# Optimization experiments

Hardware: AMD Instinct MI355X
Metric: run time of the kernel (lower is better)

## Reference

```python
import jax, jax.numpy as jnp
import numpy as np

N = 400_000
B = 64          # number of segments (point clouds)
IN_C = 128
INTER = (256, 512, 512)
OUT_C = 512


def setup_inputs() -> dict:
    key = jax.random.key(0)
    ks = jax.random.split(key, 12)
    pos_emd = jax.random.normal(ks[0], (N, IN_C), dtype=jnp.float32)
    radius_p_batch = jnp.sort(jax.random.randint(ks[1], (N,), 0, B))

    def lin(k, fin, fout):
        kw, kb = jax.random.split(k)
        s = 1.0 / np.sqrt(fin)
        W = jax.random.uniform(kw, (fin, fout), jnp.float32, -s, s)
        b = jax.random.uniform(kb, (fout,), jnp.float32, -s, s)
        return W, b

    W1, b1 = lin(ks[2], IN_C, INTER[0])
    W2, b2 = lin(ks[3], INTER[0], INTER[1])
    W3, b3 = lin(ks[4], INTER[1], INTER[2])
    W4, b4 = lin(ks[5], IN_C + INTER[2], OUT_C)
    W5, b5 = lin(ks[6], OUT_C, OUT_C)
    return {
        "pos_emd": pos_emd, "radius_p_batch": radius_p_batch,
        "W1": W1, "b1": b1, "W2": W2, "b2": b2, "W3": W3, "b3": b3,
        "W4": W4, "b4": b4, "W5": W5, "b5": b5,
    }


def reference(pos_emd, radius_p_batch, W1, b1, W2, b2, W3, b3, W4, b4, W5, b5):
    # mlp1: Linear-ReLU-Linear-ReLU-Linear
    h = jax.nn.relu(pos_emd @ W1 + b1)
    h = jax.nn.relu(h @ W2 + b2)
    h = h @ W3 + b3                              # [N, 512]
    # global max pool over segments
    g = jax.ops.segment_max(h, radius_p_batch, num_segments=B)  # [B, 512]
    # broadcast each segment's global feature back to its points (ids sorted)
    g_rep = g[radius_p_batch]                    # [N, 512]
    z = jnp.concatenate((pos_emd, g_rep), axis=-1)  # [N, 640]
    # mlp2: Linear-ReLU-Linear
    z = jax.nn.relu(z @ W4 + b4)
    z = z @ W5 + b5                              # [N, 512]
    return jax.ops.segment_max(z, radius_p_batch, num_segments=B)  # [B, 512]
```

## Files before the change

kernel.cpp:

```cpp
#include <hip/hip_runtime.h>
#include <stdint.h>


typedef __bf16 bf16;
typedef __bf16 bf16x4 __attribute__((ext_vector_type(4)));
typedef __bf16 bf16x8 __attribute__((ext_vector_type(8)));
typedef float f32x4 __attribute__((ext_vector_type(4)));

#define N_PTS 400000
#define ORD_NEG_INF 0x007FFFFFu

__device__ __forceinline__ unsigned f2ord(float f) {
  unsigned u = __float_as_uint(f);
  return (u & 0x80000000u) ? ~u : (u | 0x80000000u);
}
__device__ __forceinline__ float ord2f(unsigned o) {
  unsigned u = (o & 0x80000000u) ? (o ^ 0x80000000u) : ~o;
  return __uint_as_float(u);
}

__device__ __forceinline__ void gld16(const bf16* g, bf16* l) {
  __builtin_amdgcn_global_load_lds((const __attribute__((address_space(1))) void*)g,
                                   (__attribute__((address_space(3))) void*)l, 16, 0, 0);
}

__global__ void k_init(unsigned* g_ord, unsigned* out_u) {
  int i = blockIdx.x * 256 + threadIdx.x;
  if (i < 64 * 512) { g_ord[i] = ORD_NEG_INF; out_u[i] = ORD_NEG_INF; }
}

__global__ void k_convX(const float* __restrict__ x, bf16* __restrict__ y, long n4) {
  long i = (long)blockIdx.x * 256 + threadIdx.x;
  long stride = (long)gridDim.x * 256;
  for (; i < n4; i += stride) {
    float4 v = ((const float4*)x)[i];
    bf16x4 o = {(bf16)v.x, (bf16)v.y, (bf16)v.z, (bf16)v.w};
    ((bf16x4*)y)[i] = o;
  }
}

__global__ void k_convWt(const float* __restrict__ W, bf16* __restrict__ Wt, int K, int Nout) {
  int idx = blockIdx.x * 256 + threadIdx.x;
  if (idx < K * Nout) {
    int k = idx / Nout, c = idx - k * Nout;
    Wt[(size_t)c * K + k] = (bf16)W[idx];
  }
}

__global__ void k_segbias(const unsigned* __restrict__ g_ord, const float* __restrict__ W4,
                          const float* __restrict__ b4, float* __restrict__ sb) {
  const int s = blockIdx.x, c = threadIdx.x;
  __shared__ float gs[512];
  gs[c] = ord2f(g_ord[s * 512 + c]);
  __syncthreads();
  float acc = b4[c];
  for (int j = 0; j < 512; ++j) acc = fmaf(gs[j], W4[(size_t)(128 + j) * 512 + c], acc);
  sb[s * 512 + c] = acc;
}

__global__ void k_decode(unsigned* p, int n) {
  int i = blockIdx.x * 256 + threadIdx.x;
  if (i < n) { float f = ord2f(p[i]); ((float*)p)[i] = f; }
}

template <int BIASMODE, bool RELU, int EPI, int K, int NOUT>
__launch_bounds__(256)
__global__ void k_gemm(const bf16* __restrict__ A, const bf16* __restrict__ Bt,
                       const float* __restrict__ bias, const int* __restrict__ ids,
                       long row_off, bf16* __restrict__ out,
                       unsigned* __restrict__ outAtomic) {
  constexpr int KT = K / 32;
  constexpr int NBX = NOUT / 128;
  __shared__ __align__(16) bf16 sA[2][4096];
  __shared__ __align__(16) bf16 sB[2][4096];
  __shared__ int sIds[128];
  const int tid = threadIdx.x;
  const int wid = tid >> 6, lane = tid & 63;

  const int nwg = NBX * (int)gridDim.y;
  const int orig = (int)blockIdx.y * NBX + (int)blockIdx.x;
  const int q = nwg >> 3, r = nwg & 7;
  const int xcd = orig & 7, lid = orig >> 3;
  const int wg = (xcd < r ? xcd * (q + 1) : r * (q + 1) + (xcd - r) * q) + lid;
  const int n0 = (wg % NBX) * 128;
  const int m0 = (wg / NBX) * 128;

  if ((BIASMODE == 1 || EPI == 1) && tid < 128) sIds[tid] = ids[row_off + m0 + tid];

  const int c0 = wid * 64 + lane;
  const int srow = c0 >> 2;
  const int schunk = (c0 & 3) ^ ((c0 >> 3) & 3);
  const bf16* gA0 = A + (size_t)(m0 + srow) * K + schunk * 8;
  const bf16* gA1 = gA0 + (size_t)64 * K;
  const bf16* gB0 = Bt + (size_t)(n0 + srow) * K + schunk * 8;
  const bf16* gB1 = gB0 + (size_t)64 * K;
  bf16* sA0 = &sA[0][0];
  bf16* sB0 = &sB[0][0];

  auto STAGE = [&](int b, int kt) {
    const int ko = kt * 32;
    bf16* la = sA0 + b * 4096 + wid * 512;
    bf16* lb = sB0 + b * 4096 + wid * 512;
    gld16(gA0 + ko, la); gld16(gA1 + ko, la + 2048);
    gld16(gB0 + ko, lb); gld16(gB1 + ko, lb + 2048);
  };

  const int wr = wid >> 1, wc = wid & 1;
  const int lr = lane & 15, lk = lane >> 4;
  const int swz = (lr >> 1) & 3;
  const int foA = (wr * 64 + lr) * 32 + ((lk ^ swz) * 8);
  const int foB = (wc * 64 + lr) * 32 + ((lk ^ swz) * 8);

  f32x4 acc[4][4];
#pragma unroll
  for (int i = 0; i < 4; ++i)
#pragma unroll
    for (int j = 0; j < 4; ++j) acc[i][j] = {0.f, 0.f, 0.f, 0.f};

  STAGE(0, 0);
  if (KT > 1) STAGE(1, 1);

#pragma unroll 1
  for (int kt = 0; kt < KT - 1; ++kt) {
    asm volatile("s_waitcnt vmcnt(4)" ::: "memory");
    __syncthreads();
    const bf16* pa = sA0 + (kt & 1) * 4096 + foA;
    const bf16* pb = sB0 + (kt & 1) * 4096 + foB;
    bf16x8 af[4], bfr[4];
#pragma unroll
    for (int i = 0; i < 4; ++i) af[i] = *(const bf16x8*)(pa + i * 512);
#pragma unroll
    for (int i = 0; i < 4; ++i) bfr[i] = *(const bf16x8*)(pb + i * 512);
    asm volatile("s_waitcnt lgkmcnt(0)" ::: "memory");
    __syncthreads();
    if (kt + 2 < KT) STAGE(kt & 1, kt + 2);
#pragma unroll
    for (int i = 0; i < 4; ++i)
#pragma unroll
      for (int j = 0; j < 4; ++j)
        acc[i][j] = __builtin_amdgcn_mfma_f32_16x16x32_bf16(af[i], bfr[j], acc[i][j], 0, 0, 0);
  }
  {
    asm volatile("s_waitcnt vmcnt(0)" ::: "memory");
    __syncthreads();
    const bf16* pa = sA0 + ((KT - 1) & 1) * 4096 + foA;
    const bf16* pb = sB0 + ((KT - 1) & 1) * 4096 + foB;
    bf16x8 af[4], bfr[4];
#pragma unroll
    for (int i = 0; i < 4; ++i) af[i] = *(const bf16x8*)(pa + i * 512);
#pragma unroll
    for (int i = 0; i < 4; ++i) bfr[i] = *(const bf16x8*)(pb + i * 512);
#pragma unroll
    for (int i = 0; i < 4; ++i)
#pragma unroll
      for (int j = 0; j < 4; ++j)
        acc[i][j] = __builtin_amdgcn_mfma_f32_16x16x32_bf16(af[i], bfr[j], acc[i][j], 0, 0, 0);
  }

  if constexpr (EPI == 0) {
#pragma unroll
    for (int j = 0; j < 4; ++j) {
      const int col = n0 + wc * 64 + j * 16 + lr;
      float bcol = (BIASMODE == 0) ? bias[col] : 0.f;
#pragma unroll
      for (int i = 0; i < 4; ++i) {
#pragma unroll
        for (int q2 = 0; q2 < 4; ++q2) {
          const int rl = wr * 64 + i * 16 + lk * 4 + q2;
          float v = acc[i][j][q2];
          if constexpr (BIASMODE == 0) v += bcol;
          else v += bias[(size_t)sIds[rl] * 512 + col];
          if constexpr (RELU) v = fmaxf(v, 0.f);
          out[(size_t)(m0 + rl) * NOUT + col] = (bf16)v;
        }
      }
    }
  } else {
    const int sLo = sIds[wr * 64], sHi = sIds[wr * 64 + 63];
#pragma unroll
    for (int j = 0; j < 4; ++j) {
      const int col = n0 + wc * 64 + j * 16 + lr;
      const float bcol = bias[col];
      for (int s = sLo; s <= sHi; ++s) {
        float m = -__builtin_inff();
#pragma unroll
        for (int i = 0; i < 4; ++i)
#pragma unroll
          for (int q2 = 0; q2 < 4; ++q2) {
            const int rl = wr * 64 + i * 16 + lk * 4 + q2;
            float v = acc[i][j][q2] + bcol;
            m = (sIds[rl] == s) ? fmaxf(m, v) : m;
          }
        m = fmaxf(m, __shfl_xor(m, 16));
        m = fmaxf(m, __shfl_xor(m, 32));
        if (lane < 16) atomicMax(&outAtomic[(size_t)s * 512 + col], f2ord(m));
      }
    }
  }
}

static inline long lmin(long a, long b) { return a < b ? a : b; }

extern "C" void kernel_launch(void* const* d_in, const int* in_sizes, int n_in,
                              void* d_out, int out_size, void* d_ws, size_t ws_size,
                              hipStream_t stream) {
  const float* pos = (const float*)d_in[0];
  const int* ids = (const int*)d_in[1];
  const float* W1 = (const float*)d_in[2]; const float* b1 = (const float*)d_in[3];
  const float* W2 = (const float*)d_in[4]; const float* b2 = (const float*)d_in[5];
  const float* W3 = (const float*)d_in[6]; const float* b3 = (const float*)d_in[7];
  const float* W4 = (const float*)d_in[8]; const float* b4 = (const float*)d_in[9];
  const float* W5 = (const float*)d_in[10]; const float* b5 = (const float*)d_in[11];

  char* ws = (char*)d_ws;
  size_t off = 0;
  auto alloc = [&](size_t bytes) -> char* {
    off = (off + 255) & ~(size_t)255;
    char* p = ws + off; off += bytes; return p;
  };
  bf16* Wt1  = (bf16*)alloc(128 * 256 * 2);
  bf16* Wt2  = (bf16*)alloc(256 * 512 * 2);
  bf16* Wt3  = (bf16*)alloc(512 * 512 * 2);
  bf16* Wt4a = (bf16*)alloc(128 * 512 * 2);
  bf16* Wt5  = (bf16*)alloc(512 * 512 * 2);
  unsigned* g_ord = (unsigned*)alloc(64 * 512 * 4);
  float* sb = (float*)alloc(64 * 512 * 4);

  const size_t per_row = (128 + 256 + 512) * 2;
  size_t fixed_end = (off + 255) & ~(size_t)255;
  long avail = (long)ws_size - (long)fixed_end - 8192;
  long chunk = (avail / (long)per_row) & ~127L;
  if (chunk > N_PTS) chunk = N_PTS;
  if (chunk < 128) chunk = 128;

  bf16* Xbf = (bf16*)alloc((size_t)chunk * 128 * 2);
  bf16* h1  = (bf16*)alloc((size_t)chunk * 256 * 2);
  bf16* h2  = (bf16*)alloc((size_t)chunk * 512 * 2);

  const int nChunks = (int)((N_PTS + chunk - 1) / chunk);

  k_init<<<dim3(128), dim3(256), 0, stream>>>(g_ord, (unsigned*)d_out);
  k_convWt<<<dim3((128 * 256 + 255) / 256), dim3(256), 0, stream>>>(W1, Wt1, 128, 256);
  k_convWt<<<dim3((256 * 512 + 255) / 256), dim3(256), 0, stream>>>(W2, Wt2, 256, 512);
  k_convWt<<<dim3((512 * 512 + 255) / 256), dim3(256), 0, stream>>>(W3, Wt3, 512, 512);
  k_convWt<<<dim3((128 * 512 + 255) / 256), dim3(256), 0, stream>>>(W4, Wt4a, 128, 512);
  k_convWt<<<dim3((512 * 512 + 255) / 256), dim3(256), 0, stream>>>(W5, Wt5, 512, 512);

  for (long o = 0; o < N_PTS; o += chunk) {
    long rows = lmin(chunk, N_PTS - o);
    long n4 = rows * 32;
    long cb = lmin(2048, (n4 + 255) / 256);
    k_convX<<<dim3((unsigned)cb), dim3(256), 0, stream>>>(pos + o * 128, Xbf, n4);
    unsigned mb = (unsigned)(rows / 128);
    k_gemm<0, true, 0, 128, 256><<<dim3(2, mb), dim3(256), 0, stream>>>(Xbf, Wt1, b1, ids, o, h1, nullptr);
    k_gemm<0, true, 0, 256, 512><<<dim3(4, mb), dim3(256), 0, stream>>>(h1, Wt2, b2, ids, o, h2, nullptr);
    k_gemm<0, false, 1, 512, 512><<<dim3(4, mb), dim3(256), 0, stream>>>(h2, Wt3, b3, ids, o, nullptr, g_ord);
  }
  k_segbias<<<dim3(64), dim3(512), 0, stream>>>(g_ord, W4, b4, sb);
  for (long o = 0; o < N_PTS; o += chunk) {
    long rows = lmin(chunk, N_PTS - o);
    if (nChunks > 1) {
      long n4 = rows * 32;
      long cb = lmin(2048, (n4 + 255) / 256);
      k_convX<<<dim3((unsigned)cb), dim3(256), 0, stream>>>(pos + o * 128, Xbf, n4);
    }
    unsigned mb = (unsigned)(rows / 128);
    k_gemm<1, true, 0, 128, 512><<<dim3(4, mb), dim3(256), 0, stream>>>(Xbf, Wt4a, sb, ids, o, h2, nullptr);
    k_gemm<0, false, 1, 512, 512><<<dim3(4, mb), dim3(256), 0, stream>>>(h2, Wt5, b5, ids, o, nullptr, (unsigned*)d_out);
  }
  k_decode<<<dim3(128), dim3(256), 0, stream>>>((unsigned*)d_out, 64 * 512);
}
```

Before: 1.308 ms.

## Enlarge GEMM tiles to 256x256 with 8 waves and 4-stage LDS pipeline

The bf16 MFMA GEMM moves from a 128x128 tile with 4 waves and double buffering to a 256x256 tile with 8 waves (each 128x64), a 4-deep global-to-LDS ring and s_setprio around the MFMA blocks. The larger tile is meant to raise arithmetic intensity and cut redundant global/LDS traffic, and the deeper prefetch is meant to hide load latency with one barrier pair per k-step. It adds padding and row-validity handling for a partial last tile, and uses 128 KB of LDS per block, which limits occupancy and leaves fewer workgroups for the 400k-row problem.

After: 1.373 ms. 1.05x slower.

```diff
diff --git a/kernel.cpp b/kernel.cpp
--- a/kernel.cpp
+++ b/kernel.cpp
@@ -64,97 +64,98 @@
 }
 
 template <int BIASMODE, bool RELU, int EPI, int K, int NOUT>
-__launch_bounds__(256)
+__launch_bounds__(512, 2)
 __global__ void k_gemm(const bf16* __restrict__ A, const bf16* __restrict__ Bt,
                        const float* __restrict__ bias, const int* __restrict__ ids,
                        long row_off, bf16* __restrict__ out,
                        unsigned* __restrict__ outAtomic) {
   constexpr int KT = K / 32;
-  constexpr int NBX = NOUT / 128;
-  __shared__ __align__(16) bf16 sA[2][4096];
-  __shared__ __align__(16) bf16 sB[2][4096];
-  __shared__ int sIds[128];
+  constexpr int NBX = NOUT / 256;
+  __shared__ __align__(16) bf16 sAll[4][2][8192];
+  __shared__ int sIds[256];
   const int tid = threadIdx.x;
   const int wid = tid >> 6, lane = tid & 63;
+  const int wr = wid >> 2, wc = wid & 3;
+  const int lr = lane & 15, lk = lane >> 4;
 
   const int nwg = NBX * (int)gridDim.y;
   const int orig = (int)blockIdx.y * NBX + (int)blockIdx.x;
   const int q = nwg >> 3, r = nwg & 7;
   const int xcd = orig & 7, lid = orig >> 3;
   const int wg = (xcd < r ? xcd * (q + 1) : r * (q + 1) + (xcd - r) * q) + lid;
-  const int n0 = (wg % NBX) * 128;
-  const int m0 = (wg / NBX) * 128;
-
-  if ((BIASMODE == 1 || EPI == 1) && tid < 128) sIds[tid] = ids[row_off + m0 + tid];
-
-  const int c0 = wid * 64 + lane;
-  const int srow = c0 >> 2;
-  const int schunk = (c0 & 3) ^ ((c0 >> 3) & 3);
-  const bf16* gA0 = A + (size_t)(m0 + srow) * K + schunk * 8;
-  const bf16* gA1 = gA0 + (size_t)64 * K;
-  const bf16* gB0 = Bt + (size_t)(n0 + srow) * K + schunk * 8;
-  const bf16* gB1 = gB0 + (size_t)64 * K;
-  bf16* sA0 = &sA[0][0];
-  bf16* sB0 = &sB[0][0];
-
-  auto STAGE = [&](int b, int kt) {
+  const int n0 = (wg % NBX) * 256;
+  const int m0 = (wg / NBX) * 256;
+
+  if constexpr (BIASMODE == 1 || EPI == 1) {
+    if (tid < 256) {
+      long gi = row_off + m0 + tid;
+      if (gi > (long)N_PTS - 1) gi = (long)N_PTS - 1;
+      sIds[tid] = ids[gi];
+    }
+  }
+
+  const int rg0 = wid * 2;
+  const int ssr = lane >> 2;
+  const int scb = ((lane & 3) >> 1) ^ ((lane >> 5) & 1);
+  const int csrc = scb * 16 + (lane & 1) * 8;
+  const bf16* gA = A + (size_t)(m0 + rg0 * 16 + ssr) * K + csrc;
+  const bf16* gB = Bt + (size_t)(n0 + rg0 * 16 + ssr) * K + csrc;
+
+  auto STAGE = [&](int kt) {
+    const int b = kt & 3;
     const int ko = kt * 32;
-    bf16* la = sA0 + b * 4096 + wid * 512;
-    bf16* lb = sB0 + b * 4096 + wid * 512;
-    gld16(gA0 + ko, la); gld16(gA1 + ko, la + 2048);
-    gld16(gB0 + ko, lb); gld16(gB1 + ko, lb + 2048);
+    bf16* la = &sAll[b][0][rg0 * 512];
+    bf16* lb = &sAll[b][1][rg0 * 512];
+    gld16(gA + ko, la);
+    gld16(gA + (size_t)16 * K + ko, la + 512);
+    gld16(gB + ko, lb);
+    gld16(gB + (size_t)16 * K + ko, lb + 512);
   };
 
-  const int wr = wid >> 1, wc = wid & 1;
-  const int lr = lane & 15, lk = lane >> 4;
-  const int swz = (lr >> 1) & 3;
-  const int foA = (wr * 64 + lr) * 32 + ((lk ^ swz) * 8);
-  const int foB = (wc * 64 + lr) * 32 + ((lk ^ swz) * 8);
-
-  f32x4 acc[4][4];
-#pragma unroll
-  for (int i = 0; i < 4; ++i)
+  const int cread = (lk * 8) ^ ((lr & 8) ? 16 : 0);
+  const int foA = (wr * 8) * 512 + lr * 32 + cread;
+  const int foB = (wc * 4) * 512 + lr * 32 + cread;
+
+  f32x4 acc[8][4];
+#pragma unroll
+  for (int i = 0; i < 8; ++i)
 #pragma unroll
     for (int j = 0; j < 4; ++j) acc[i][j] = {0.f, 0.f, 0.f, 0.f};
 
-  STAGE(0, 0);
-  if (KT > 1) STAGE(1, 1);
+  STAGE(0); STAGE(1); STAGE(2);
 
 #pragma unroll 1
-  for (int kt = 0; kt < KT - 1; ++kt) {
-    asm volatile("s_waitcnt vmcnt(4)" ::: "memory");
+  for (int kt = 0; kt < KT; ++kt) {
+    const int b = kt & 3;
+    if (kt <= KT - 3) asm volatile("s_waitcnt vmcnt(8)" ::: "memory");
+    else if (kt == KT - 2) asm volatile("s_waitcnt vmcnt(4)" ::: "memory");
+    else asm volatile("s_waitcnt vmcnt(0)" ::: "memory");
     __syncthreads();
-    const bf16* pa = sA0 + (kt & 1) * 4096 + foA;
-    const bf16* pb = sB0 + (kt & 1) * 4096 + foB;
-    bf16x8 af[4], bfr[4];
-#pragma unroll
-    for (int i = 0; i < 4; ++i) af[i] = *(const bf16x8*)(pa + i * 512);
-#pragma unroll
-    for (int i = 0; i < 4; ++i) bfr[i] = *(const bf16x8*)(pb + i * 512);
-    asm volatile("s_waitcnt lgkmcnt(0)" ::: "memory");
-    __syncthreads();
-    if (kt + 2 < KT) STAGE(kt & 1, kt + 2);
+    if (kt <= KT - 4) STAGE(kt + 3);
+    const bf16* Ab = &sAll[b][0][0];
+    const bf16* Bb = &sAll[b][1][0];
+    bf16x8 bfr[4], af[4];
+#pragma unroll
+    for (int j = 0; j < 4; ++j) bfr[j] = *(const bf16x8*)(Bb + foB + j * 512);
+#pragma unroll
+    for (int i = 0; i < 4; ++i) af[i] = *(const bf16x8*)(Ab + foA + i * 512);
+    __builtin_amdgcn_s_setprio(1);
 #pragma unroll
     for (int i = 0; i < 4; ++i)
 #pragma unroll
       for (int j = 0; j < 4; ++j)
         acc[i][j] = __builtin_amdgcn_mfma_f32_16x16x32_bf16(af[i], bfr[j], acc[i][j], 0, 0, 0);
-  }
-  {
-    asm volatile("s_waitcnt vmcnt(0)" ::: "memory");
+    __builtin_amdgcn_s_setprio(0);
     __syncthreads();
-    const bf16* pa = sA0 + ((KT - 1) & 1) * 4096 + foA;
-    const bf16* pb = sB0 + ((KT - 1) & 1) * 4096 + foB;
-    bf16x8 af[4], bfr[4];
-#pragma unroll
-    for (int i = 0; i < 4; ++i) af[i] = *(const bf16x8*)(pa + i * 512);
-#pragma unroll
-    for (int i = 0; i < 4; ++i) bfr[i] = *(const bf16x8*)(pb + i * 512);
+#pragma unroll
+    for (int i = 0; i < 4; ++i) af[i] = *(const bf16x8*)(Ab + foA + (4 + i) * 512);
+    __builtin_amdgcn_s_setprio(1);
 #pragma unroll
     for (int i = 0; i < 4; ++i)
 #pragma unroll
       for (int j = 0; j < 4; ++j)
-        acc[i][j] = __builtin_amdgcn_mfma_f32_16x16x32_bf16(af[i], bfr[j], acc[i][j], 0, 0, 0);
+        acc[4 + i][j] = __builtin_amdgcn_mfma_f32_16x16x32_bf16(af[i], bfr[j], acc[4 + i][j], 0, 0, 0);
+    __builtin_amdgcn_s_setprio(0);
   }
 
   if constexpr (EPI == 0) {
@@ -163,10 +164,10 @@
       const int col = n0 + wc * 64 + j * 16 + lr;
       float bcol = (BIASMODE == 0) ? bias[col] : 0.f;
 #pragma unroll
-      for (int i = 0; i < 4; ++i) {
+      for (int i = 0; i < 8; ++i) {
 #pragma unroll
         for (int q2 = 0; q2 < 4; ++q2) {
-          const int rl = wr * 64 + i * 16 + lk * 4 + q2;
+          const int rl = wr * 128 + i * 16 + lk * 4 + q2;
           float v = acc[i][j][q2];
           if constexpr (BIASMODE == 0) v += bcol;
           else v += bias[(size_t)sIds[rl] * 512 + col];
@@ -176,7 +177,7 @@
       }
     }
   } else {
-    const int sLo = sIds[wr * 64], sHi = sIds[wr * 64 + 63];
+    const int sLo = sIds[wr * 128], sHi = sIds[wr * 128 + 127];
 #pragma unroll
     for (int j = 0; j < 4; ++j) {
       const int col = n0 + wc * 64 + j * 16 + lr;
@@ -184,12 +185,13 @@
       for (int s = sLo; s <= sHi; ++s) {
         float m = -__builtin_inff();
 #pragma unroll
-        for (int i = 0; i < 4; ++i)
+        for (int i = 0; i < 8; ++i)
 #pragma unroll
           for (int q2 = 0; q2 < 4; ++q2) {
-            const int rl = wr * 64 + i * 16 + lk * 4 + q2;
+            const int rl = wr * 128 + i * 16 + lk * 4 + q2;
+            const bool rv = (row_off + m0 + rl) < (long)N_PTS;
             float v = acc[i][j][q2] + bcol;
-            m = (sIds[rl] == s) ? fmaxf(m, v) : m;
+            m = (sIds[rl] == s && rv) ? fmaxf(m, v) : m;
           }
         m = fmaxf(m, __shfl_xor(m, 16));
         m = fmaxf(m, __shfl_xor(m, 32));
@@ -229,13 +231,15 @@
   const size_t per_row = (128 + 256 + 512) * 2;
   size_t fixed_end = (off + 255) & ~(size_t)255;
   long avail = (long)ws_size - (long)fixed_end - 8192;
-  long chunk = (avail / (long)per_row) & ~127L;
+  long maxrows = avail / (long)per_row;
+  long chunk = (maxrows - 256) & ~255L;
   if (chunk > N_PTS) chunk = N_PTS;
-  if (chunk < 128) chunk = 128;
-
-  bf16* Xbf = (bf16*)alloc((size_t)chunk * 128 * 2);
-  bf16* h1  = (bf16*)alloc((size_t)chunk * 256 * 2);
-  bf16* h2  = (bf16*)alloc((size_t)chunk * 512 * 2);
+  if (chunk < 256) chunk = 256;
+  long rows_alloc = chunk + 256;
+
+  bf16* Xbf = (bf16*)alloc((size_t)rows_alloc * 128 * 2);
+  bf16* h1  = (bf16*)alloc((size_t)rows_alloc * 256 * 2);
+  bf16* h2  = (bf16*)alloc((size_t)rows_alloc * 512 * 2);
 
   const int nChunks = (int)((N_PTS + chunk - 1) / chunk);
 
@@ -251,10 +255,10 @@
     long n4 = rows * 32;
     long cb = lmin(2048, (n4 + 255) / 256);
     k_convX<<<dim3((unsigned)cb), dim3(256), 0, stream>>>(pos + o * 128, Xbf, n4);
-    unsigned mb = (unsigned)(rows / 128);
-    k_gemm<0, true, 0, 128, 256><<<dim3(2, mb), dim3(256), 0, stream>>>(Xbf, Wt1, b1, ids, o, h1, nullptr);
-    k_gemm<0, true, 0, 256, 512><<<dim3(4, mb), dim3(256), 0, stream>>>(h1, Wt2, b2, ids, o, h2, nullptr);
-    k_gemm<0, false, 1, 512, 512><<<dim3(4, mb), dim3(256), 0, stream>>>(h2, Wt3, b3, ids, o, nullptr, g_ord);
+    unsigned mb = (unsigned)((rows + 255) / 256);
+    k_gemm<0, true, 0, 128, 256><<<dim3(1, mb), dim3(512), 0, stream>>>(Xbf, Wt1, b1, ids, o, h1, nullptr);
+    k_gemm<0, true, 0, 256, 512><<<dim3(2, mb), dim3(512), 0, stream>>>(h1, Wt2, b2, ids, o, h2, nullptr);
+    k_gemm<0, false, 1, 512, 512><<<dim3(2, mb), dim3(512), 0, stream>>>(h2, Wt3, b3, ids, o, nullptr, g_ord);
   }
   k_segbias<<<dim3(64), dim3(512), 0, stream>>>(g_ord, W4, b4, sb);
   for (long o = 0; o < N_PTS; o += chunk) {
@@ -264,9 +268,9 @@
       long cb = lmin(2048, (n4 + 255) / 256);
       k_convX<<<dim3((unsigned)cb), dim3(256), 0, stream>>>(pos + o * 128, Xbf, n4);
     }
-    unsigned mb = (unsigned)(rows / 128);
-    k_gemm<1, true, 0, 128, 512><<<dim3(4, mb), dim3(256), 0, stream>>>(Xbf, Wt4a, sb, ids, o, h2, nullptr);
-    k_gemm<0, false, 1, 512, 512><<<dim3(4, mb), dim3(256), 0, stream>>>(h2, Wt5, b5, ids, o, nullptr, (unsigned*)d_out);
+    unsigned mb = (unsigned)((rows + 255) / 256);
+    k_gemm<1, true, 0, 128, 512><<<dim3(2, mb), dim3(512), 0, stream>>>(Xbf, Wt4a, sb, ids, o, h2, nullptr);
+    k_gemm<0, false, 1, 512, 512><<<dim3(2, mb), dim3(512), 0, stream>>>(h2, Wt5, b5, ids, o, nullptr, (unsigned*)d_out);
   }
   k_decode<<<dim3(128), dim3(256), 0, stream>>>((unsigned*)d_out, 64 * 512);
 }
```
